# Kernel tuning notes

Hardware: AMD Instinct MI355X
Metric: run time of the kernel (lower is better)

Reference implementation:

```python
import jax, jax.numpy as jnp
import numpy as np

V = 163842  # ico6 sphere vertex count
C_IN = 64
C_OUT = 64


def setup_inputs() -> dict:
    key = jax.random.key(0)
    k1, k2, k3, k4 = jax.random.split(key, 4)
    x = jax.random.normal(k1, (2, V, C_IN), dtype=jnp.float32)
    neigh_orders = jax.random.randint(k2, (V * 7,), 0, V, dtype=jnp.int64)
    W = jax.random.normal(k3, (C_OUT, 7 * C_IN), dtype=jnp.float32) * 0.05
    b = jax.random.normal(k4, (C_OUT,), dtype=jnp.float32) * 0.05
    return {"x": x, "neigh_orders": neigh_orders, "W": W, "b": b}


def reference(x, neigh_orders, W, b):
    B, Vn, C = x.shape
    # gather 7 neighbors per vertex: (B, V*7, C) -> (B, V, 7*C)
    mat = x[:, neigh_orders].reshape(B, Vn, 7 * C)
    # Linear: mat @ W.T + b -> (B, V, C_out)
    return jnp.einsum('bvk,ok->bvo', mat, W) + b
```

## Files before the change

kernel.cpp:

```cpp
#include <hip/hip_runtime.h>


constexpr int V_ICO   = 163842;
constexpr int C       = 64;
constexpr int KTOT    = 448;
constexpr int M_TOTAL = 2 * V_ICO;
constexpr int X_ELEMS = M_TOTAL * C;
constexpr int W_ELEMS = C * KTOT;
constexpr int XCH     = X_ELEMS / 8;
constexpr int WCH     = W_ELEMS / 8;

typedef __attribute__((ext_vector_type(4))) float          f32x4;
typedef __attribute__((ext_vector_type(4))) unsigned int   u32x4;
typedef __attribute__((ext_vector_type(8))) unsigned short u16x8;
typedef __attribute__((ext_vector_type(8))) __bf16         bf16x8;

union BF8 { u32x4 q; u16x8 u; bf16x8 v; };

static __device__ __forceinline__ unsigned short f2bf(float f) {
  unsigned int t = __float_as_uint(f);
  t += 0x7FFFu + ((t >> 16) & 1u);
  return (unsigned short)(t >> 16);
}

static __device__ __forceinline__ u32x4 cvt8(f32x4 a, f32x4 b) {
  BF8 r;
  r.u[0] = f2bf(a[0]); r.u[1] = f2bf(a[1]); r.u[2] = f2bf(a[2]); r.u[3] = f2bf(a[3]);
  r.u[4] = f2bf(b[0]); r.u[5] = f2bf(b[1]); r.u[6] = f2bf(b[2]); r.u[7] = f2bf(b[3]);
  return r.q;
}

__global__ __launch_bounds__(256)
void cvt_x_w(const float* __restrict__ x, const float* __restrict__ W,
             u32x4* __restrict__ xbf, u32x4* __restrict__ wbf) {
  const int stride = gridDim.x * blockDim.x;
  for (int i = blockIdx.x * blockDim.x + threadIdx.x; i < XCH + WCH; i += stride) {
    const f32x4* src;
    u32x4* dst;
    if (i < XCH) {
      src = reinterpret_cast<const f32x4*>(x) + 2 * (size_t)i;
      dst = xbf + i;
    } else {
      const int k = i - XCH;
      src = reinterpret_cast<const f32x4*>(W) + 2 * (size_t)k;
      dst = wbf + k;
    }
    f32x4 f0 = src[0], f1 = src[1];
    *dst = cvt8(f0, f1);
  }
}

__global__ __launch_bounds__(256)
void cvt_w_only(const float* __restrict__ W, u32x4* __restrict__ wbf) {
  const int i = blockIdx.x * blockDim.x + threadIdx.x;
  if (i < WCH) {
    const f32x4* src = reinterpret_cast<const f32x4*>(W) + 2 * (size_t)i;
    f32x4 f0 = src[0], f1 = src[1];
    wbf[i] = cvt8(f0, f1);
  }
}

template <int XBF, int WPRE>
__global__ __launch_bounds__(512, 4)
void gather_mm(const float* __restrict__ x32, const unsigned short* __restrict__ x16,
               const int* __restrict__ neigh,
               const float* __restrict__ W32, const unsigned short* __restrict__ W16,
               const float* __restrict__ bias, float* __restrict__ out) {
  __shared__ __align__(16) unsigned short Wlds[64][456];

  const int tid = threadIdx.x;
  for (int i = tid; i < 64 * 56; i += 512) {
    const int row = i / 56, ch = i - row * 56;
    u32x4 val;
    if constexpr (WPRE) {
      val = reinterpret_cast<const u32x4*>(W16)[i];
    } else {
      const f32x4* p = reinterpret_cast<const f32x4*>(W32 + row * 448 + ch * 8);
      val = cvt8(p[0], p[1]);
    }
    *reinterpret_cast<u32x4*>(&Wlds[row][ch * 8]) = val;
  }
  __syncthreads();

  const int w    = tid >> 6;
  const int lane = tid & 63;
  const int r    = lane & 15;
  const int g    = lane >> 4;
  const int m0   = blockIdx.x * 128 + w * 16;
  if (m0 >= M_TOTAL) return;

  int mA = m0 + r;
  if (mA > M_TOTAL - 1) mA = M_TOTAL - 1;
  const int bA = (mA >= V_ICO) ? 1 : 0;
  const int vA = mA - bA * V_ICO;

  int nofs[7];
#pragma unroll
  for (int j = 0; j < 7; ++j) nofs[j] = neigh[vA * 7 + j];

  const unsigned short* xb16 = nullptr;
  const float* xb32 = nullptr;
  if constexpr (XBF) xb16 = x16 + (size_t)bA * V_ICO * 64;
  else               xb32 = x32 + (size_t)bA * V_ICO * 64;

  const f32x4 zero = {0.f, 0.f, 0.f, 0.f};
  f32x4 acc[4] = {zero, zero, zero, zero};

#pragma unroll
  for (int kc = 0; kc < 14; ++kc) {
    const int j  = kc >> 1;
    const int c0 = ((kc & 1) << 5) | (g << 3);
    BF8 a;
    if constexpr (XBF) {
      a.q = *reinterpret_cast<const u32x4*>(xb16 + (size_t)nofs[j] * 64 + c0);
    } else {
      const f32x4* p = reinterpret_cast<const f32x4*>(xb32 + (size_t)nofs[j] * 64 + c0);
      a.q = cvt8(p[0], p[1]);
    }
    const int kb = kc * 32 + (g << 3);
    const bf16x8* pb0 = reinterpret_cast<const bf16x8*>(&Wlds[r][kb]);
    const bf16x8* pb1 = reinterpret_cast<const bf16x8*>(&Wlds[16 + r][kb]);
    const bf16x8* pb2 = reinterpret_cast<const bf16x8*>(&Wlds[32 + r][kb]);
    const bf16x8* pb3 = reinterpret_cast<const bf16x8*>(&Wlds[48 + r][kb]);
    acc[0] = __builtin_amdgcn_mfma_f32_16x16x32_bf16(a.v, *pb0, acc[0], 0, 0, 0);
    acc[1] = __builtin_amdgcn_mfma_f32_16x16x32_bf16(a.v, *pb1, acc[1], 0, 0, 0);
    acc[2] = __builtin_amdgcn_mfma_f32_16x16x32_bf16(a.v, *pb2, acc[2], 0, 0, 0);
    acc[3] = __builtin_amdgcn_mfma_f32_16x16x32_bf16(a.v, *pb3, acc[3], 0, 0, 0);
  }

#pragma unroll
  for (int nt = 0; nt < 4; ++nt) {
    const int o = (nt << 4) + r;
    const float bv = bias[o];
#pragma unroll
    for (int q2 = 0; q2 < 4; ++q2) {
      const int mS = m0 + (g << 2) + q2;
      if (mS < M_TOTAL) out[(size_t)mS * 64 + o] = acc[nt][q2] + bv;
    }
  }
}

extern "C" void kernel_launch(void* const* d_in, const int* in_sizes, int n_in,
                              void* d_out, int out_size, void* d_ws, size_t ws_size,
                              hipStream_t stream) {
  const float* x    = (const float*)d_in[0];
  const int*   nbr  = (const int*)d_in[1];
  const float* W    = (const float*)d_in[2];
  const float* bias = (const float*)d_in[3];
  float* out = (float*)d_out;

  const size_t xbf_bytes = (size_t)X_ELEMS * 2;
  const size_t wbf_bytes = (size_t)W_ELEMS * 2;
  const int grid_main = (M_TOTAL + 127) / 128;

  if (ws_size >= xbf_bytes + wbf_bytes) {
    u32x4* xbf = (u32x4*)d_ws;
    u32x4* wbf = (u32x4*)((char*)d_ws + xbf_bytes);
    hipLaunchKernelGGL(cvt_x_w, dim3(2048), dim3(256), 0, stream, x, W, xbf, wbf);
    hipLaunchKernelGGL((gather_mm<1, 1>), dim3(grid_main), dim3(512), 0, stream,
                       x, (const unsigned short*)xbf, nbr,
                       W, (const unsigned short*)wbf, bias, out);
  } else if (ws_size >= wbf_bytes) {
    u32x4* wbf = (u32x4*)d_ws;
    hipLaunchKernelGGL(cvt_w_only, dim3((WCH + 255) / 256), dim3(256), 0, stream, W, wbf);
    hipLaunchKernelGGL((gather_mm<0, 1>), dim3(grid_main), dim3(512), 0, stream,
                       x, nullptr, nbr, W, (const unsigned short*)wbf, bias, out);
  } else {
    hipLaunchKernelGGL((gather_mm<0, 0>), dim3(grid_main), dim3(512), 0, stream,
                       x, nullptr, nbr, W, nullptr, bias, out);
  }
}
```

Measured before the change: 223.1 us.

## Double-buffer neighbor loads, enlarge blocks, and use nontemporal stores

```diff
diff --git a/kernel.cpp b/kernel.cpp
--- a/kernel.cpp
+++ b/kernel.cpp
@@ -2,11 +2,9 @@
 
 
 constexpr int V_ICO   = 163842;
-constexpr int C       = 64;
-constexpr int KTOT    = 448;
 constexpr int M_TOTAL = 2 * V_ICO;
-constexpr int X_ELEMS = M_TOTAL * C;
-constexpr int W_ELEMS = C * KTOT;
+constexpr int X_ELEMS = M_TOTAL * 64;
+constexpr int W_ELEMS = 64 * 448;
 constexpr int XCH     = X_ELEMS / 8;
 constexpr int WCH     = W_ELEMS / 8;
 
@@ -33,21 +31,20 @@
 __global__ __launch_bounds__(256)
 void cvt_x_w(const float* __restrict__ x, const float* __restrict__ W,
              u32x4* __restrict__ xbf, u32x4* __restrict__ wbf) {
-  const int stride = gridDim.x * blockDim.x;
-  for (int i = blockIdx.x * blockDim.x + threadIdx.x; i < XCH + WCH; i += stride) {
-    const f32x4* src;
-    u32x4* dst;
-    if (i < XCH) {
-      src = reinterpret_cast<const f32x4*>(x) + 2 * (size_t)i;
-      dst = xbf + i;
-    } else {
-      const int k = i - XCH;
-      src = reinterpret_cast<const f32x4*>(W) + 2 * (size_t)k;
-      dst = wbf + k;
-    }
-    f32x4 f0 = src[0], f1 = src[1];
-    *dst = cvt8(f0, f1);
+  const int i = blockIdx.x * blockDim.x + threadIdx.x;
+  if (i >= XCH + WCH) return;
+  const f32x4* src;
+  u32x4* dst;
+  if (i < XCH) {
+    src = reinterpret_cast<const f32x4*>(x) + 2 * (size_t)i;
+    dst = xbf + i;
+  } else {
+    const int k = i - XCH;
+    src = reinterpret_cast<const f32x4*>(W) + 2 * (size_t)k;
+    dst = wbf + k;
   }
+  f32x4 f0 = src[0], f1 = src[1];
+  __builtin_nontemporal_store(cvt8(f0, f1), dst);
 }
 
 __global__ __launch_bounds__(256)
@@ -61,7 +58,7 @@
 }
 
 template <int XBF, int WPRE>
-__global__ __launch_bounds__(512, 4)
+__global__ __launch_bounds__(1024, 8)
 void gather_mm(const float* __restrict__ x32, const unsigned short* __restrict__ x16,
                const int* __restrict__ neigh,
                const float* __restrict__ W32, const unsigned short* __restrict__ W16,
@@ -69,7 +66,7 @@
   __shared__ __align__(16) unsigned short Wlds[64][456];
 
   const int tid = threadIdx.x;
-  for (int i = tid; i < 64 * 56; i += 512) {
+  for (int i = tid; i < 64 * 56; i += 1024) {
     const int row = i / 56, ch = i - row * 56;
     u32x4 val;
     if constexpr (WPRE) {
@@ -86,7 +83,7 @@
   const int lane = tid & 63;
   const int r    = lane & 15;
   const int g    = lane >> 4;
-  const int m0   = blockIdx.x * 128 + w * 16;
+  const int m0   = blockIdx.x * 256 + w * 16;
   if (m0 >= M_TOTAL) return;
 
   int mA = m0 + r;
@@ -98,44 +95,68 @@
 #pragma unroll
   for (int j = 0; j < 7; ++j) nofs[j] = neigh[vA * 7 + j];
 
-  const unsigned short* xb16 = nullptr;
+  const unsigned short* xb = nullptr;
   const float* xb32 = nullptr;
-  if constexpr (XBF) xb16 = x16 + (size_t)bA * V_ICO * 64;
-  else               xb32 = x32 + (size_t)bA * V_ICO * 64;
+  if constexpr (XBF) xb   = x16 + (size_t)bA * V_ICO * 64 + (g << 3);
+  else               xb32 = x32 + (size_t)bA * V_ICO * 64 + (g << 3);
+
+  const unsigned short* wp = &Wlds[r][g << 3];
 
   const f32x4 zero = {0.f, 0.f, 0.f, 0.f};
-  f32x4 acc[4] = {zero, zero, zero, zero};
+  f32x4 acc0 = zero, acc1 = zero, acc2 = zero, acc3 = zero;
 
+#define LOAD_J(d0, d1, j) do {                                              \
+    if constexpr (XBF) {                                                    \
+      const unsigned short* rp = xb + (size_t)nofs[j] * 64;                 \
+      d0.q = *reinterpret_cast<const u32x4*>(rp);                           \
+      d1.q = *reinterpret_cast<const u32x4*>(rp + 32);                      \
+    } else {                                                                \
+      const float* rp = xb32 + (size_t)nofs[j] * 64;                        \
+      const f32x4* p0 = reinterpret_cast<const f32x4*>(rp);                 \
+      const f32x4* p1 = reinterpret_cast<const f32x4*>(rp + 32);            \
+      d0.q = cvt8(p0[0], p0[1]);                                            \
+      d1.q = cvt8(p1[0], p1[1]);                                            \
+    }                                                                       \
+  } while (0)
+
+#define MFMA_NT(afrag, nt, kc)                                              \
+    acc##nt = __builtin_amdgcn_mfma_f32_16x16x32_bf16(                      \
+        afrag.v,                                                            \
+        *reinterpret_cast<const bf16x8*>(wp + (nt) * 16 * 456 + (kc) * 32), \
+        acc##nt, 0, 0, 0)
+
+#define COMPUTE_J(d0, d1, j) do {                                           \
+    MFMA_NT(d0, 0, 2*(j));   MFMA_NT(d0, 1, 2*(j));                         \
+    MFMA_NT(d0, 2, 2*(j));   MFMA_NT(d0, 3, 2*(j));                         \
+    MFMA_NT(d1, 0, 2*(j)+1); MFMA_NT(d1, 1, 2*(j)+1);                       \
+    MFMA_NT(d1, 2, 2*(j)+1); MFMA_NT(d1, 3, 2*(j)+1);                       \
+  } while (0)
+
+  BF8 a0lo, a0hi, a1lo, a1hi;
+  LOAD_J(a0lo, a0hi, 0);
+  LOAD_J(a1lo, a1hi, 1);
+  COMPUTE_J(a0lo, a0hi, 0); LOAD_J(a0lo, a0hi, 2);
+  COMPUTE_J(a1lo, a1hi, 1); LOAD_J(a1lo, a1hi, 3);
+  COMPUTE_J(a0lo, a0hi, 2); LOAD_J(a0lo, a0hi, 4);
+  COMPUTE_J(a1lo, a1hi, 3); LOAD_J(a1lo, a1hi, 5);
+  COMPUTE_J(a0lo, a0hi, 4); LOAD_J(a0lo, a0hi, 6);
+  COMPUTE_J(a1lo, a1hi, 5);
+  COMPUTE_J(a0lo, a0hi, 6);
+
+#undef LOAD_J
+#undef MFMA_NT
+#undef COMPUTE_J
+
+  const float bv0 = bias[r], bv1 = bias[16 + r], bv2 = bias[32 + r], bv3 = bias[48 + r];
 #pragma unroll
-  for (int kc = 0; kc < 14; ++kc) {
-    const int j  = kc >> 1;
-    const int c0 = ((kc & 1) << 5) | (g << 3);
-    BF8 a;
-    if constexpr (XBF) {
-      a.q = *reinterpret_cast<const u32x4*>(xb16 + (size_t)nofs[j] * 64 + c0);
-    } else {
-      const f32x4* p = reinterpret_cast<const f32x4*>(xb32 + (size_t)nofs[j] * 64 + c0);
-      a.q = cvt8(p[0], p[1]);
-    }
-    const int kb = kc * 32 + (g << 3);
-    const bf16x8* pb0 = reinterpret_cast<const bf16x8*>(&Wlds[r][kb]);
-    const bf16x8* pb1 = reinterpret_cast<const bf16x8*>(&Wlds[16 + r][kb]);
-    const bf16x8* pb2 = reinterpret_cast<const bf16x8*>(&Wlds[32 + r][kb]);
-    const bf16x8* pb3 = reinterpret_cast<const bf16x8*>(&Wlds[48 + r][kb]);
-    acc[0] = __builtin_amdgcn_mfma_f32_16x16x32_bf16(a.v, *pb0, acc[0], 0, 0, 0);
-    acc[1] = __builtin_amdgcn_mfma_f32_16x16x32_bf16(a.v, *pb1, acc[1], 0, 0, 0);
-    acc[2] = __builtin_amdgcn_mfma_f32_16x16x32_bf16(a.v, *pb2, acc[2], 0, 0, 0);
-    acc[3] = __builtin_amdgcn_mfma_f32_16x16x32_bf16(a.v, *pb3, acc[3], 0, 0, 0);
-  }
-
-#pragma unroll
-  for (int nt = 0; nt < 4; ++nt) {
-    const int o = (nt << 4) + r;
-    const float bv = bias[o];
-#pragma unroll
-    for (int q2 = 0; q2 < 4; ++q2) {
-      const int mS = m0 + (g << 2) + q2;
-      if (mS < M_TOTAL) out[(size_t)mS * 64 + o] = acc[nt][q2] + bv;
+  for (int q2 = 0; q2 < 4; ++q2) {
+    const int mS = m0 + (g << 2) + q2;
+    if (mS < M_TOTAL) {
+      float* o = out + (size_t)mS * 64;
+      __builtin_nontemporal_store(acc0[q2] + bv0, o + r);
+      __builtin_nontemporal_store(acc1[q2] + bv1, o + 16 + r);
+      __builtin_nontemporal_store(acc2[q2] + bv2, o + 32 + r);
+      __builtin_nontemporal_store(acc3[q2] + bv3, o + 48 + r);
     }
   }
 }
@@ -151,22 +172,23 @@
 
   const size_t xbf_bytes = (size_t)X_ELEMS * 2;
   const size_t wbf_bytes = (size_t)W_ELEMS * 2;
-  const int grid_main = (M_TOTAL + 127) / 128;
+  const int grid_main = (M_TOTAL + 255) / 256;
 
   if (ws_size >= xbf_bytes + wbf_bytes) {
     u32x4* xbf = (u32x4*)d_ws;
     u32x4* wbf = (u32x4*)((char*)d_ws + xbf_bytes);
-    hipLaunchKernelGGL(cvt_x_w, dim3(2048), dim3(256), 0, stream, x, W, xbf, wbf);
-    hipLaunchKernelGGL((gather_mm<1, 1>), dim3(grid_main), dim3(512), 0, stream,
+    hipLaunchKernelGGL(cvt_x_w, dim3((XCH + WCH + 255) / 256), dim3(256), 0, stream,
+                       x, W, xbf, wbf);
+    hipLaunchKernelGGL((gather_mm<1, 1>), dim3(grid_main), dim3(1024), 0, stream,
                        x, (const unsigned short*)xbf, nbr,
                        W, (const unsigned short*)wbf, bias, out);
   } else if (ws_size >= wbf_bytes) {
     u32x4* wbf = (u32x4*)d_ws;
     hipLaunchKernelGGL(cvt_w_only, dim3((WCH + 255) / 256), dim3(256), 0, stream, W, wbf);
-    hipLaunchKernelGGL((gather_mm<0, 1>), dim3(grid_main), dim3(512), 0, stream,
+    hipLaunchKernelGGL((gather_mm<0, 1>), dim3(grid_main), dim3(1024), 0, stream,
                        x, nullptr, nbr, W, (const unsigned short*)wbf, bias, out);
   } else {
-    hipLaunchKernelGGL((gather_mm<0, 0>), dim3(grid_main), dim3(512), 0, stream,
+    hipLaunchKernelGGL((gather_mm<0, 0>), dim3(grid_main), dim3(1024), 0, stream,
                        x, nullptr, nbr, W, nullptr, bias, out);
   }
 }
```

Measured after the change: 207.6 us. 1.07x faster.
